# Performance work log

Measured on AMD Instinct MI355X. Metric: run time of the kernel, lower is better.

The kernel has to match this reference:

```python
import jax, jax.numpy as jnp
import numpy as np

N_USER = 100000
N_ITEM = 50000
D = 128
E = 600000
LN_EPS = 1e-5
NEG_SLOPE = 0.01  # torch nn.LeakyReLU default


def setup_inputs() -> dict:
    key = jax.random.key(0)
    ks = jax.random.split(key, 8)
    scale = 1.0 / np.sqrt(D)
    return {
        "x_user": jax.random.normal(ks[0], (N_USER, D), jnp.float32),
        "x_item": jax.random.normal(ks[1], (N_ITEM, D), jnp.float32),
        "W_ui": jax.random.normal(ks[2], (D, D), jnp.float32) * scale,
        "b_ui": jnp.zeros((D,), jnp.float32),
        "W_iu": jax.random.normal(ks[3], (D, D), jnp.float32) * scale,
        "b_iu": jnp.zeros((D,), jnp.float32),
        "ln_w_user": jnp.ones((D,), jnp.float32),
        "ln_b_user": jnp.zeros((D,), jnp.float32),
        "ln_w_item": jnp.ones((D,), jnp.float32),
        "ln_b_item": jnp.zeros((D,), jnp.float32),
        "edge_src_ui": jax.random.randint(ks[4], (E,), 0, N_USER, jnp.int32),
        "edge_dst_ui": jax.random.randint(ks[5], (E,), 0, N_ITEM, jnp.int32),
        "edge_src_iu": jax.random.randint(ks[6], (E,), 0, N_ITEM, jnp.int32),
        "edge_dst_iu": jax.random.randint(ks[7], (E,), 0, N_USER, jnp.int32),
    }


def _ngcf_conv(x_src, x_dst, W, b, src_idx, dst_idx, num_dst):
    # message: LeakyReLU(Linear(x_j * x_i)) per edge, then scatter-add at dst
    m = jax.nn.leaky_relu((x_src[src_idx] * x_dst[dst_idx]) @ W + b, NEG_SLOPE)
    return jax.ops.segment_sum(m, dst_idx, num_segments=num_dst)


def _node_layernorm(x, w, b):
    # PyG LayerNorm(mode='node'): normalize each node over feature dim
    mu = jnp.mean(x, axis=-1, keepdims=True)
    var = jnp.mean(jnp.square(x - mu), axis=-1, keepdims=True)
    return (x - mu) * jax.lax.rsqrt(var + LN_EPS) * w + b


def reference(x_user, x_item, W_ui, b_ui, W_iu, b_iu,
              ln_w_user, ln_b_user, ln_w_item, ln_b_item,
              edge_src_ui, edge_dst_ui, edge_src_iu, edge_dst_iu):
    # HeteroConv with aggr='sum' (single relation per destination type here)
    agg_item = _ngcf_conv(x_user, x_item, W_ui, b_ui, edge_src_ui, edge_dst_ui, N_ITEM)
    agg_user = _ngcf_conv(x_item, x_user, W_iu, b_iu, edge_src_iu, edge_dst_iu, N_USER)
    out_user = jax.nn.relu(_node_layernorm(agg_user, ln_w_user, ln_b_user))
    out_item = jax.nn.relu(_node_layernorm(agg_item, ln_w_item, ln_b_item))
    return out_user, out_item
```

## Files before the change

### kernel.cpp

```cpp
#include <hip/hip_runtime.h>
#include <stdint.h>

#define D 128
#define E_EDGES 600000
#define E2 1200000
#define N_USER_C 100000
#define N_ITEM_C 50000
#define NSEG_TOT 150000
#define NCPAD 150528
#define NSCAN_BLOCKS 147
#define NEG_SLOPE 0.01f
#define LN_EPS 1e-5f

#define GRID_BLOCKS 1280
#define HIST_BLOCKS ((E2 + 255) / 256)
#define CVT_BLOCKS 1024

typedef __attribute__((ext_vector_type(8))) _Float16 f16x8;
typedef __attribute__((ext_vector_type(4))) float f32x4;
typedef __attribute__((ext_vector_type(2))) float f32x2;

__global__ void prep_k(const int* __restrict__ edst_ui, const int* __restrict__ edst_iu,
                       int* __restrict__ counts,
                       const float* __restrict__ xu, const float* __restrict__ xi,
                       _Float16* __restrict__ xuh, _Float16* __restrict__ xih,
                       _Float16* __restrict__ zrow) {
    const int b = blockIdx.x;
    if (b < HIST_BLOCKS) {
        int e = b * 256 + threadIdx.x;
        if (e < E_EDGES)      atomicAdd(&counts[edst_ui[e]], 1);
        else if (e < E2)      atomicAdd(&counts[N_ITEM_C + edst_iu[e - E_EDGES]], 1);
    } else {
        int tid = (b - HIST_BLOCKS) * 256 + threadIdx.x;
        if (tid < 32) ((uint2*)zrow)[tid] = (uint2){0u, 0u};
        const int NU4 = N_USER_C * 32;
        const int NT4 = NU4 + N_ITEM_C * 32;
        for (int v = tid; v < NT4; v += CVT_BLOCKS * 256) {
            const bool isu = v < NU4;
            const float4 f = isu ? ((const float4*)xu)[v] : ((const float4*)xi)[v - NU4];
            _Float16* o = isu ? (xuh + (size_t)v * 4) : (xih + (size_t)(v - NU4) * 4);
            uint2 p;
            p.x = __builtin_bit_cast(uint32_t, __builtin_amdgcn_cvt_pkrtz(f.x, f.y));
            p.y = __builtin_bit_cast(uint32_t, __builtin_amdgcn_cvt_pkrtz(f.z, f.w));
            *(uint2*)o = p;
        }
    }
}

__global__ void scan_block_k(const int* __restrict__ counts, int* __restrict__ offsets,
                             int* __restrict__ partial, int n) {
    __shared__ int sm[1024];
    const int t = threadIdx.x;
    const int i = blockIdx.x * 1024 + t;
    int v = (i < n) ? counts[i] : 0;
    sm[t] = v;
    __syncthreads();
    for (int off = 1; off < 1024; off <<= 1) {
        int x = (t >= off) ? sm[t - off] : 0;
        __syncthreads();
        sm[t] += x;
        __syncthreads();
    }
    if (i < n) offsets[i] = sm[t] - v;
    if (t == 1023) partial[blockIdx.x] = sm[t];
}

__global__ void scan_part_k(int* __restrict__ partial, int nb) {
    __shared__ int sm[256];
    const int t = threadIdx.x;
    int v = (t < nb) ? partial[t] : 0;
    sm[t] = v;
    __syncthreads();
    for (int off = 1; off < 256; off <<= 1) {
        int x = (t >= off) ? sm[t - off] : 0;
        __syncthreads();
        sm[t] += x;
        __syncthreads();
    }
    if (t < nb) partial[t] = sm[t] - v;
}

__global__ void scan_add_k(int* __restrict__ offsets, const int* __restrict__ partial,
                           int* __restrict__ counts, int n) {
    const int i = blockIdx.x * 1024 + threadIdx.x;
    if (i < n) {
        offsets[i] += partial[blockIdx.x];
        counts[i] = 0;
    }
}

__global__ void scatter_k(const int* __restrict__ esrc_ui, const int* __restrict__ edst_ui,
                          const int* __restrict__ esrc_iu, const int* __restrict__ edst_iu,
                          const int* __restrict__ offsets, int* __restrict__ counts,
                          int* __restrict__ sorted) {
    int e = blockIdx.x * 256 + threadIdx.x;
    int s, c;
    if (e < E_EDGES)      { s = esrc_ui[e];            c = edst_ui[e]; }
    else if (e < E2)      { s = esrc_iu[e - E_EDGES];  c = N_ITEM_C + edst_iu[e - E_EDGES]; }
    else return;
    int pos = offsets[c] + atomicAdd(&counts[c], 1);
    sorted[pos] = s;
}

__global__ __launch_bounds__(256, 2) void conv_k(
    const _Float16* __restrict__ xsh, const _Float16* __restrict__ xdh,
    const float* __restrict__ Wp, const float* __restrict__ bp,
    const float* __restrict__ lnw, const float* __restrict__ lnb,
    const int* __restrict__ offsets, const int* __restrict__ sorted,
    const _Float16* __restrict__ zrow, float* __restrict__ outp,
    int n_dst, int cbase)
{
    __shared__ _Float16 WtF[32 * 64 * 8];

    const int t = threadIdx.x;
    for (int idx = t; idx < 2048; idx += 256) {
        const int frag = idx >> 6, lane = idx & 63;
        const int n = frag >> 2, kt = frag & 3;
        const int col = n * 16 + (lane & 15);
        const int k0  = kt * 32 + (lane >> 4) * 8;
        f16x8 v;
        #pragma unroll
        for (int e = 0; e < 8; e++) v[e] = (_Float16)Wp[(k0 + e) * 128 + col];
        *(f16x8*)&WtF[idx * 8] = v;
    }
    __syncthreads();

    const int l    = t & 63;
    const int lo16 = l & 15;
    const int quad = l >> 4;
    const int n0 = 2 * quad, n1 = n0 + 1;
    const int col0 = n0 * 16 + lo16, col1 = n1 * 16 + lo16;

    float bn[8];
    #pragma unroll
    for (int n = 0; n < 8; n++) bn[n] = bp[n * 16 + lo16];
    const float lw0 = lnw[col0], lw1 = lnw[col1];
    const float lb0 = lnb[col0], lb1 = lnb[col1];

    const int stride = GRID_BLOCKS * 4;
    int d = blockIdx.x * 4 + (t >> 6);

    int st_c = offsets[cbase + d];
    int en_c = (cbase + d + 1 < NSEG_TOT) ? offsets[cbase + d + 1] : E2;
    int idx_c = sorted[st_c + lo16];

    while (d < n_dst) {
        const int dn = d + stride;
        int st_n = 0, en_n = 0, idx_n = 0;
        if (dn < n_dst) {
            st_n = offsets[cbase + dn];
            en_n = (cbase + dn + 1 < NSEG_TOT) ? offsets[cbase + dn + 1] : E2;
            idx_n = sorted[st_n + lo16];
        }
        const int start = st_c;
        const int len   = en_c - st_c;

        const f16x8* pdh = (const f16x8*)(xdh + ((size_t)d << 7));
        f16x8 dr[4];
        #pragma unroll
        for (int kt = 0; kt < 4; kt++) dr[kt] = pdh[kt * 4 + quad];

        float nacc[8];
        #pragma unroll
        for (int n = 0; n < 8; n++) nacc[n] = 0.f;

        const int lim = len > 0 ? len : 1;
        for (int c0i = 0; c0i < lim; c0i += 16) {
            const int sj = (c0i == 0) ? idx_c : sorted[start + c0i + lo16];
            const bool okg = (c0i + lo16) < len;
            const f16x8* ps = okg ? (const f16x8*)(xsh + ((size_t)sj << 7))
                                  : (const f16x8*)zrow;
            f16x8 af[4];
            #pragma unroll
            for (int kt = 0; kt < 4; kt++) af[kt] = ps[kt * 4 + quad] * dr[kt];

            #pragma unroll
            for (int h = 0; h < 2; h++) {
                f32x4 acc[4];
                #pragma unroll
                for (int n = 0; n < 4; n++) {
                    const float b = bn[h * 4 + n];
                    acc[n] = (f32x4){b, b, b, b};
                }
                #pragma unroll
                for (int kt = 0; kt < 4; kt++) {
                    #pragma unroll
                    for (int n = 0; n < 4; n++) {
                        f16x8 bf = *(const f16x8*)&WtF[(((h * 4 + n) * 4 + kt) * 64 + l) * 8];
                        acc[n] = __builtin_amdgcn_mfma_f32_16x16x32_f16(af[kt], bf, acc[n], 0, 0, 0);
                    }
                }
                #pragma unroll
                for (int n = 0; n < 4; n++) {
                    f32x2 v01 = (f32x2){acc[n][0], acc[n][1]};
                    f32x2 v23 = (f32x2){acc[n][2], acc[n][3]};
                    v01 = __builtin_elementwise_max(v01, v01 * NEG_SLOPE);
                    v23 = __builtin_elementwise_max(v23, v23 * NEG_SLOPE);
                    f32x2 vv = v01 + v23;
                    nacc[h * 4 + n] += vv.x + vv.y;
                }
            }
        }

        const int nch = (lim + 15) >> 4;
        const float inv = (float)((nch << 4) - len);
        float s1 = 0.f, s2 = 0.f;
        #pragma unroll
        for (int n = 0; n < 8; n++) {
            float s = nacc[n];
            s += __shfl_xor(s, 16);
            s += __shfl_xor(s, 32);
            s -= inv * fmaxf(bn[n], NEG_SLOPE * bn[n]);
            nacc[n] = s;
            s1 += s; s2 += s * s;
        }
        #pragma unroll
        for (int off = 1; off <= 8; off <<= 1) {
            s1 += __shfl_xor(s1, off);
            s2 += __shfl_xor(s2, off);
        }
        const float mu  = s1 * (1.0f / 128.0f);
        const float var = s2 * (1.0f / 128.0f) - mu * mu;
        const float rs  = rsqrtf(var + LN_EPS);

        float o0 = (nacc[n0] - mu) * rs * lw0 + lb0;
        float o1 = (nacc[n1] - mu) * rs * lw1 + lb1;
        float* rp = outp + ((size_t)d << 7);
        rp[col0] = fmaxf(o0, 0.f);
        rp[col1] = fmaxf(o1, 0.f);

        st_c = st_n; en_c = en_n; idx_c = idx_n;
        d = dn;
    }
}


extern "C" void kernel_launch(void* const* d_in, const int* in_sizes, int n_in,
                              void* d_out, int out_size, void* d_ws, size_t ws_size,
                              hipStream_t stream) {
    const float* x_user    = (const float*)d_in[0];
    const float* x_item    = (const float*)d_in[1];
    const float* W_ui      = (const float*)d_in[2];
    const float* b_ui      = (const float*)d_in[3];
    const float* W_iu      = (const float*)d_in[4];
    const float* b_iu      = (const float*)d_in[5];
    const float* ln_w_user = (const float*)d_in[6];
    const float* ln_b_user = (const float*)d_in[7];
    const float* ln_w_item = (const float*)d_in[8];
    const float* ln_b_item = (const float*)d_in[9];
    const int* esrc_ui = (const int*)d_in[10];
    const int* edst_ui = (const int*)d_in[11];
    const int* esrc_iu = (const int*)d_in[12];
    const int* edst_iu = (const int*)d_in[13];

    float* out = (float*)d_out;
    float* out_user = out;
    float* out_item = out + (size_t)N_USER_C * D;

    int* counts  = (int*)d_ws;
    int* offsets = counts + NCPAD;
    int* partial = offsets + NCPAD;
    int* sorted  = partial + 256;
    _Float16* zrow = (_Float16*)(sorted + E2 + 16);
    _Float16* xuh  = zrow + 256;
    _Float16* xih  = xuh + (size_t)N_USER_C * D;

    hipMemsetAsync(counts, 0, (size_t)NCPAD * sizeof(int), stream);

    prep_k<<<dim3(HIST_BLOCKS + CVT_BLOCKS), dim3(256), 0, stream>>>(
        edst_ui, edst_iu, counts, x_user, x_item, xuh, xih, zrow);

    scan_block_k<<<dim3(NSCAN_BLOCKS), dim3(1024), 0, stream>>>(counts, offsets, partial, NCPAD);
    scan_part_k<<<dim3(1), dim3(256), 0, stream>>>(partial, NSCAN_BLOCKS);
    scan_add_k<<<dim3(NSCAN_BLOCKS), dim3(1024), 0, stream>>>(offsets, partial, counts, NCPAD);

    scatter_k<<<dim3(HIST_BLOCKS), dim3(256), 0, stream>>>(
        esrc_ui, edst_ui, esrc_iu, edst_iu, offsets, counts, sorted);

    conv_k<<<dim3(GRID_BLOCKS), dim3(256), 0, stream>>>(
        xuh, xih, W_ui, b_ui, ln_w_item, ln_b_item,
        offsets, sorted, zrow, out_item, N_ITEM_C, 0);
    conv_k<<<dim3(GRID_BLOCKS), dim3(256), 0, stream>>>(
        xih, xuh, W_iu, b_iu, ln_w_user, ln_b_user,
        offsets, sorted, zrow, out_user, N_USER_C, N_ITEM_C);
}
```

Baseline: 536.9 us.

## Fuse scan into single-pass lookback kernel and merge both conv launches

Result: faster. 517.7 us (-3.6%).

```diff
diff --git a/kernel.cpp b/kernel.cpp
--- a/kernel.cpp
+++ b/kernel.cpp
@@ -12,7 +12,8 @@
 #define NEG_SLOPE 0.01f
 #define LN_EPS 1e-5f
 
-#define GRID_BLOCKS 1280
+#define CONV_BLOCKS 1280
+#define ITEM_BLOCKS 480
 #define HIST_BLOCKS ((E2 + 255) / 256)
 #define CVT_BLOCKS 1024
 
@@ -21,7 +22,7 @@
 typedef __attribute__((ext_vector_type(2))) float f32x2;
 
 __global__ void prep_k(const int* __restrict__ edst_ui, const int* __restrict__ edst_iu,
-                       int* __restrict__ counts,
+                       int* __restrict__ counts, int* __restrict__ totals,
                        const float* __restrict__ xu, const float* __restrict__ xi,
                        _Float16* __restrict__ xuh, _Float16* __restrict__ xih,
                        _Float16* __restrict__ zrow) {
@@ -32,7 +33,10 @@
         else if (e < E2)      atomicAdd(&counts[N_ITEM_C + edst_iu[e - E_EDGES]], 1);
     } else {
         int tid = (b - HIST_BLOCKS) * 256 + threadIdx.x;
-        if (tid < 32) ((uint2*)zrow)[tid] = (uint2){0u, 0u};
+        if (b == HIST_BLOCKS) {
+            if (threadIdx.x < 160) totals[threadIdx.x] = -1;
+            if (threadIdx.x < 32) ((uint2*)zrow)[threadIdx.x] = (uint2){0u, 0u};
+        }
         const int NU4 = N_USER_C * 32;
         const int NT4 = NU4 + N_ITEM_C * 32;
         for (int v = tid; v < NT4; v += CVT_BLOCKS * 256) {
@@ -47,12 +51,14 @@
     }
 }
 
-__global__ void scan_block_k(const int* __restrict__ counts, int* __restrict__ offsets,
-                             int* __restrict__ partial, int n) {
+__global__ void scan_full_k(int* __restrict__ counts, int* __restrict__ offsets,
+                            int* __restrict__ totals) {
     __shared__ int sm[1024];
+    __shared__ int psum;
     const int t = threadIdx.x;
-    const int i = blockIdx.x * 1024 + t;
-    int v = (i < n) ? counts[i] : 0;
+    const int b = blockIdx.x;
+    const int i = b * 1024 + t;
+    const int v = counts[i];
     sm[t] = v;
     __syncthreads();
     for (int off = 1; off < 1024; off <<= 1) {
@@ -61,32 +67,21 @@
         sm[t] += x;
         __syncthreads();
     }
-    if (i < n) offsets[i] = sm[t] - v;
-    if (t == 1023) partial[blockIdx.x] = sm[t];
-}
-
-__global__ void scan_part_k(int* __restrict__ partial, int nb) {
-    __shared__ int sm[256];
-    const int t = threadIdx.x;
-    int v = (t < nb) ? partial[t] : 0;
-    sm[t] = v;
-    __syncthreads();
-    for (int off = 1; off < 256; off <<= 1) {
-        int x = (t >= off) ? sm[t - off] : 0;
-        __syncthreads();
-        sm[t] += x;
-        __syncthreads();
-    }
-    if (t < nb) partial[t] = sm[t] - v;
-}
-
-__global__ void scan_add_k(int* __restrict__ offsets, const int* __restrict__ partial,
-                           int* __restrict__ counts, int n) {
-    const int i = blockIdx.x * 1024 + threadIdx.x;
-    if (i < n) {
-        offsets[i] += partial[blockIdx.x];
-        counts[i] = 0;
-    }
+    const int incl = sm[t];
+    if (t == 1023)
+        __hip_atomic_store(&totals[b], incl, __ATOMIC_RELEASE, __HIP_MEMORY_SCOPE_AGENT);
+    if (t == 0) psum = 0;
+    __syncthreads();
+    if (t < b) {
+        int x;
+        do {
+            x = __hip_atomic_load(&totals[t], __ATOMIC_ACQUIRE, __HIP_MEMORY_SCOPE_AGENT);
+        } while (x < 0);
+        atomicAdd(&psum, x);
+    }
+    __syncthreads();
+    offsets[i] = incl - v + psum;
+    counts[i] = 0;
 }
 
 __global__ void scatter_k(const int* __restrict__ esrc_ui, const int* __restrict__ edst_ui,
@@ -102,15 +97,30 @@
     sorted[pos] = s;
 }
 
-__global__ __launch_bounds__(256, 2) void conv_k(
-    const _Float16* __restrict__ xsh, const _Float16* __restrict__ xdh,
-    const float* __restrict__ Wp, const float* __restrict__ bp,
-    const float* __restrict__ lnw, const float* __restrict__ lnb,
+__global__ __launch_bounds__(256, 2) void conv2_k(
+    const _Float16* __restrict__ xuh, const _Float16* __restrict__ xih,
+    const float* __restrict__ W_ui, const float* __restrict__ b_ui,
+    const float* __restrict__ W_iu, const float* __restrict__ b_iu,
+    const float* __restrict__ lnw_u, const float* __restrict__ lnb_u,
+    const float* __restrict__ lnw_i, const float* __restrict__ lnb_i,
     const int* __restrict__ offsets, const int* __restrict__ sorted,
-    const _Float16* __restrict__ zrow, float* __restrict__ outp,
-    int n_dst, int cbase)
+    const _Float16* __restrict__ zrow,
+    float* __restrict__ out_user, float* __restrict__ out_item)
 {
     __shared__ _Float16 WtF[32 * 64 * 8];
+
+    const int rel   = blockIdx.x >= ITEM_BLOCKS;
+    const int bid_r = rel ? (blockIdx.x - ITEM_BLOCKS) : blockIdx.x;
+    const int nblk  = rel ? (CONV_BLOCKS - ITEM_BLOCKS) : ITEM_BLOCKS;
+    const _Float16* __restrict__ xsh = rel ? xih : xuh;
+    const _Float16* __restrict__ xdh = rel ? xuh : xih;
+    const float* __restrict__ Wp   = rel ? W_iu : W_ui;
+    const float* __restrict__ bp   = rel ? b_iu : b_ui;
+    const float* __restrict__ lnw  = rel ? lnw_u : lnw_i;
+    const float* __restrict__ lnb  = rel ? lnb_u : lnb_i;
+    float* __restrict__ outp       = rel ? out_user : out_item;
+    const int n_dst = rel ? N_USER_C : N_ITEM_C;
+    const int cbase = rel ? N_ITEM_C : 0;
 
     const int t = threadIdx.x;
     for (int idx = t; idx < 2048; idx += 256) {
@@ -137,11 +147,11 @@
     const float lw0 = lnw[col0], lw1 = lnw[col1];
     const float lb0 = lnb[col0], lb1 = lnb[col1];
 
-    const int stride = GRID_BLOCKS * 4;
-    int d = blockIdx.x * 4 + (t >> 6);
+    const int stride = nblk * 4;
+    int d = bid_r * 4 + (t >> 6);
 
     int st_c = offsets[cbase + d];
-    int en_c = (cbase + d + 1 < NSEG_TOT) ? offsets[cbase + d + 1] : E2;
+    int en_c = offsets[cbase + d + 1];
     int idx_c = sorted[st_c + lo16];
 
     while (d < n_dst) {
@@ -149,7 +159,7 @@
         int st_n = 0, en_n = 0, idx_n = 0;
         if (dn < n_dst) {
             st_n = offsets[cbase + dn];
-            en_n = (cbase + dn + 1 < NSEG_TOT) ? offsets[cbase + dn + 1] : E2;
+            en_n = offsets[cbase + dn + 1];
             idx_n = sorted[st_n + lo16];
         }
         const int start = st_c;
@@ -259,8 +269,8 @@
 
     int* counts  = (int*)d_ws;
     int* offsets = counts + NCPAD;
-    int* partial = offsets + NCPAD;
-    int* sorted  = partial + 256;
+    int* totals  = offsets + NCPAD;
+    int* sorted  = totals + 256;
     _Float16* zrow = (_Float16*)(sorted + E2 + 16);
     _Float16* xuh  = zrow + 256;
     _Float16* xih  = xuh + (size_t)N_USER_C * D;
@@ -268,19 +278,15 @@
     hipMemsetAsync(counts, 0, (size_t)NCPAD * sizeof(int), stream);
 
     prep_k<<<dim3(HIST_BLOCKS + CVT_BLOCKS), dim3(256), 0, stream>>>(
-        edst_ui, edst_iu, counts, x_user, x_item, xuh, xih, zrow);
-
-    scan_block_k<<<dim3(NSCAN_BLOCKS), dim3(1024), 0, stream>>>(counts, offsets, partial, NCPAD);
-    scan_part_k<<<dim3(1), dim3(256), 0, stream>>>(partial, NSCAN_BLOCKS);
-    scan_add_k<<<dim3(NSCAN_BLOCKS), dim3(1024), 0, stream>>>(offsets, partial, counts, NCPAD);
+        edst_ui, edst_iu, counts, totals, x_user, x_item, xuh, xih, zrow);
+
+    scan_full_k<<<dim3(NSCAN_BLOCKS), dim3(1024), 0, stream>>>(counts, offsets, totals);
 
     scatter_k<<<dim3(HIST_BLOCKS), dim3(256), 0, stream>>>(
         esrc_ui, edst_ui, esrc_iu, edst_iu, offsets, counts, sorted);
 
-    conv_k<<<dim3(GRID_BLOCKS), dim3(256), 0, stream>>>(
-        xuh, xih, W_ui, b_ui, ln_w_item, ln_b_item,
-        offsets, sorted, zrow, out_item, N_ITEM_C, 0);
-    conv_k<<<dim3(GRID_BLOCKS), dim3(256), 0, stream>>>(
-        xih, xuh, W_iu, b_iu, ln_w_user, ln_b_user,
-        offsets, sorted, zrow, out_user, N_USER_C, N_ITEM_C);
-}
+    conv2_k<<<dim3(CONV_BLOCKS), dim3(256), 0, stream>>>(
+        xuh, xih, W_ui, b_ui, W_iu, b_iu,
+        ln_w_user, ln_b_user, ln_w_item, ln_b_item,
+        offsets, sorted, zrow, out_user, out_item);
+}
```
